# Kernel optimization log

Hardware: AMD Instinct MI355X
Metric: run time of the kernel (lower is better)

## Reference

```python
import jax, jax.numpy as jnp
import numpy as np

N, D, L, OUT, E = 50000, 64, 3, 16, 800000


def setup_inputs() -> dict:
    key = jax.random.key(0)
    ks = jax.random.split(key, 7)
    F = jax.random.normal(ks[0], (N, D), dtype=jnp.float32)
    src = jax.random.randint(ks[1], (E,), 0, N, dtype=jnp.int32)
    dst = jax.random.randint(ks[2], (E,), 0, N, dtype=jnp.int32)
    gcn_w = jax.random.normal(ks[3], (L, D, D), dtype=jnp.float32) / np.float32(np.sqrt(D))
    gcn_b = jnp.zeros((L, D), dtype=jnp.float32)
    fc_w = jax.random.normal(ks[4], (OUT, N * D), dtype=jnp.float32) / np.float32(np.sqrt(N * D))
    fc_b = jnp.zeros((OUT,), dtype=jnp.float32)
    return {"F": F, "src": src, "dst": dst, "gcn_w": gcn_w, "gcn_b": gcn_b,
            "fc_w": fc_w, "fc_b": fc_b}


def reference(F, src, dst, gcn_w, gcn_b, fc_w, fc_b):
    n = F.shape[0]
    # dgl.add_self_loop: append a self edge for every node
    loops = jnp.arange(n, dtype=src.dtype)
    s = jnp.concatenate([src, loops])
    d = jnp.concatenate([dst, loops])
    ones = jnp.ones(s.shape[0], dtype=F.dtype)
    deg_out = jax.ops.segment_sum(ones, s, num_segments=n)  # out-degree of src
    deg_in = jax.ops.segment_sum(ones, d, num_segments=n)   # in-degree of dst
    # self loops guarantee deg >= 1
    norm_src = deg_out ** -0.5
    norm_dst = deg_in ** -0.5
    x = F
    for i in range(gcn_w.shape[0]):
        h = x * norm_src[:, None]                              # [N, D]
        agg = jax.ops.segment_sum(h[s], d, num_segments=n)     # SpMM gather-scatter
        x = (agg * norm_dst[:, None]) @ gcn_w[i] + gcn_b[i]    # GraphConv norm='both'
        x = jax.nn.relu(x)
    flat = jax.nn.relu(x.reshape(-1))                          # Flatten(start_dim=0) + ReLU
    return fc_w @ flat + fc_b                                  # [OUT]
```

## Files before the change

kernel.cpp:

```cpp
#include <hip/hip_runtime.h>
#include <cstdint>

#define Nn 50000
#define Dd 64
#define Ee 800000
#define NBLK 196
#define FC_BLOCKS 512
#define ND4 (Nn*Dd/4)
#define NDTOT ((size_t)Nn * 64)

__device__ __forceinline__ float relu_f(float v){ return v > 0.f ? v : 0.f; }

__device__ __forceinline__ unsigned short f2bf(float f){
    unsigned u = __float_as_uint(f);
    u += 0x7fffu + ((u >> 16) & 1u);
    return (unsigned short)(u >> 16);
}
__device__ __forceinline__ void add_bf8(float* a, uint4 u){
    a[0] += __uint_as_float(u.x << 16);
    a[1] += __uint_as_float(u.x & 0xffff0000u);
    a[2] += __uint_as_float(u.y << 16);
    a[3] += __uint_as_float(u.y & 0xffff0000u);
    a[4] += __uint_as_float(u.z << 16);
    a[5] += __uint_as_float(u.z & 0xffff0000u);
    a[6] += __uint_as_float(u.w << 16);
    a[7] += __uint_as_float(u.w & 0xffff0000u);
}
__device__ __forceinline__ int rowidx(unsigned e, unsigned end, const unsigned* __restrict__ csr){
    unsigned ec = e < (Ee - 1u) ? e : (Ee - 1u);
    int idx = (int)csr[ec];
    return (e < end) ? idx : Nn;
}

__global__ __launch_bounds__(256) void k_degree(const int* __restrict__ src, const int* __restrict__ dst,
                                                unsigned* __restrict__ dout, unsigned* __restrict__ din){
    int e = blockIdx.x * 256 + threadIdx.x;
    if (e < Ee){
        atomicAdd(&dout[src[e]], 1u);
        atomicAdd(&din[dst[e]], 1u);
    }
}

__global__ __launch_bounds__(256) void k_blocksum(const unsigned* __restrict__ din, const unsigned* __restrict__ dout,
                                                  unsigned* __restrict__ bsum,
                                                  float* __restrict__ ns, float* __restrict__ nd){
    __shared__ unsigned s[256];
    int t = threadIdx.x; int i = blockIdx.x * 256 + t;
    unsigned v = (i < Nn) ? din[i] : 0u;
    s[t] = v;
    if (i < Nn){
        ns[i] = rsqrtf((float)(dout[i] + 1u));
        nd[i] = rsqrtf((float)(v + 1u));
    }
    __syncthreads();
    for (int off = 128; off > 0; off >>= 1){ if (t < off) s[t] += s[t + off]; __syncthreads(); }
    if (t == 0) bsum[blockIdx.x] = s[0];
}

__global__ __launch_bounds__(256) void k_scanblocks(const unsigned* __restrict__ bsum, unsigned* __restrict__ boff,
                                                    unsigned* __restrict__ offsets){
    __shared__ unsigned s[256];
    int t = threadIdx.x;
    unsigned v = (t < NBLK) ? bsum[t] : 0u;
    s[t] = v; __syncthreads();
    for (int off = 1; off < 256; off <<= 1){
        unsigned add = (t >= off) ? s[t - off] : 0u;
        __syncthreads();
        s[t] += add;
        __syncthreads();
    }
    boff[t] = s[t] - v;
    if (t == 255) offsets[Nn] = s[255];
}

__global__ __launch_bounds__(256) void k_offsets(const unsigned* __restrict__ din, const unsigned* __restrict__ boff,
                                                 unsigned* __restrict__ offsets, unsigned* __restrict__ cursor){
    __shared__ unsigned s[256];
    int t = threadIdx.x; int i = blockIdx.x * 256 + t;
    unsigned v = (i < Nn) ? din[i] : 0u;
    s[t] = v; __syncthreads();
    for (int off = 1; off < 256; off <<= 1){
        unsigned add = (t >= off) ? s[t - off] : 0u;
        __syncthreads();
        s[t] += add;
        __syncthreads();
    }
    if (i < Nn){
        unsigned val = s[t] - v + boff[blockIdx.x];
        offsets[i] = val;
        cursor[i]  = val;
    }
}

__global__ __launch_bounds__(256) void k_fillcsr(const int* __restrict__ src, const int* __restrict__ dst,
                                                 unsigned* __restrict__ cursor, unsigned* __restrict__ csr){
    int e = blockIdx.x * 256 + threadIdx.x;
    if (e < Ee){
        unsigned pos = atomicAdd(&cursor[dst[e]], 1u);
        csr[pos] = (unsigned)src[e];
    }
}

__global__ __launch_bounds__(256) void k_h0(const float* __restrict__ x, const float* __restrict__ ns,
                                            unsigned short* __restrict__ hA, unsigned short* __restrict__ hB){
    int i = blockIdx.x * 256 + threadIdx.x;
    if (i < ND4){
        const float4* x4 = (const float4*)x;
        float s = ns[i >> 4];
        float4 v = x4[i];
        ushort4 o;
        o.x = f2bf(v.x * s); o.y = f2bf(v.y * s);
        o.z = f2bf(v.z * s); o.w = f2bf(v.w * s);
        ((ushort4*)hA)[i] = o;
    } else {
        int j = i - ND4;
        if (j < 16){
            ushort4 z = make_ushort4(0, 0, 0, 0);
            ((ushort4*)hA)[ND4 + j] = z;
            ((ushort4*)hB)[ND4 + j] = z;
        }
    }
}

__global__ __launch_bounds__(256) void k_gather(const unsigned short* __restrict__ h,
                                                const unsigned* __restrict__ offsets,
                                                const unsigned* __restrict__ csr, const float* __restrict__ nd,
                                                float* __restrict__ agg){
    int v = blockIdx.x * 4 + (threadIdx.x >> 6);
    int lane = threadIdx.x & 63;
    int slot = lane >> 3;
    int sub  = lane & 7;
    const uint4* h16 = (const uint4*)h;

    unsigned beg = offsets[v], end = offsets[v + 1];
    unsigned e0 = beg + slot;

    int i0 = rowidx(e0,      end, csr);
    int i1 = rowidx(e0 + 8,  end, csr);
    int i2 = rowidx(e0 + 16, end, csr);
    int i3 = rowidx(e0 + 24, end, csr);
    uint4 u0 = h16[(size_t)i0 * 8 + sub];
    uint4 u1 = h16[(size_t)i1 * 8 + sub];
    uint4 u2 = h16[(size_t)i2 * 8 + sub];
    uint4 u3 = h16[(size_t)i3 * 8 + sub];

    float acc[8];
    #pragma unroll
    for (int i = 0; i < 8; i++) acc[i] = 0.f;
    if (slot == 0) add_bf8(acc, h16[(size_t)v * 8 + sub]);
    add_bf8(acc, u0);
    add_bf8(acc, u1);
    add_bf8(acc, u2);
    add_bf8(acc, u3);

    for (unsigned e = e0 + 32; e < end; e += 8){
        add_bf8(acc, h16[(size_t)((int)csr[e]) * 8 + sub]);
    }

    #pragma unroll
    for (int i = 0; i < 8; i++) acc[i] += __shfl_xor(acc[i], 8, 64);
    #pragma unroll
    for (int i = 0; i < 8; i++) acc[i] += __shfl_xor(acc[i], 16, 64);
    #pragma unroll
    for (int i = 0; i < 8; i++) acc[i] += __shfl_xor(acc[i], 32, 64);

    if (slot == 0){
        float s = nd[v];
        float4* aggp = (float4*)agg;
        aggp[(size_t)v * 16 + sub * 2 + 0] = make_float4(acc[0] * s, acc[1] * s, acc[2] * s, acc[3] * s);
        aggp[(size_t)v * 16 + sub * 2 + 1] = make_float4(acc[4] * s, acc[5] * s, acc[6] * s, acc[7] * s);
    }
}

__global__ __launch_bounds__(256) void k_gemm(const float* __restrict__ agg, const float* __restrict__ W,
                                              const float* __restrict__ bias, const float* __restrict__ ns,
                                              void* __restrict__ xout, int bf16_prescale_out){
    __shared__ float As[64 * 65];
    __shared__ float Ws[64 * 64];
    int t = threadIdx.x;
    int m_base = blockIdx.x * 64;
    const float4* W4   = (const float4*)W;
    float4* Ws4        = (float4*)Ws;
    const float4* agg4 = (const float4*)agg;
    #pragma unroll
    for (int i = 0; i < 4; i++){
        int g = t + 256 * i;
        Ws4[g] = W4[g];
        int m = g >> 4, q = g & 15;
        int node = m_base + m;
        float4 v = make_float4(0.f, 0.f, 0.f, 0.f);
        if (node < Nn) v = agg4[node * 16 + q];
        float* dp = &As[m * 65 + q * 4];
        dp[0] = v.x; dp[1] = v.y; dp[2] = v.z; dp[3] = v.w;
    }
    __syncthreads();
    int tm = t >> 4, tn = t & 15;
    float acc[4][4];
    #pragma unroll
    for (int i = 0; i < 4; i++)
        #pragma unroll
        for (int j = 0; j < 4; j++) acc[i][j] = 0.f;
    #pragma unroll 4
    for (int k = 0; k < 64; k++){
        float4 w = *(const float4*)&Ws[k * 64 + tn * 4];
        float a[4];
        #pragma unroll
        for (int i = 0; i < 4; i++) a[i] = As[(tm * 4 + i) * 65 + k];
        #pragma unroll
        for (int i = 0; i < 4; i++){
            acc[i][0] += a[i] * w.x;
            acc[i][1] += a[i] * w.y;
            acc[i][2] += a[i] * w.z;
            acc[i][3] += a[i] * w.w;
        }
    }
    float4 b4 = ((const float4*)bias)[tn];
    #pragma unroll
    for (int i = 0; i < 4; i++){
        int node = m_base + tm * 4 + i;
        if (node < Nn){
            float4 r;
            r.x = relu_f(acc[i][0] + b4.x);
            r.y = relu_f(acc[i][1] + b4.y);
            r.z = relu_f(acc[i][2] + b4.z);
            r.w = relu_f(acc[i][3] + b4.w);
            if (bf16_prescale_out){
                float s = ns[node];
                ushort4 o;
                o.x = f2bf(r.x * s); o.y = f2bf(r.y * s);
                o.z = f2bf(r.z * s); o.w = f2bf(r.w * s);
                ((ushort4*)xout)[node * 16 + tn] = o;
            } else {
                ((float4*)xout)[node * 16 + tn] = r;
            }
        }
    }
}

__global__ __launch_bounds__(256) void k_fc(const float* __restrict__ fcw, const float* __restrict__ x,
                                            float* __restrict__ partials){
    int t = threadIdx.x;
    const float4* x4 = (const float4*)x;
    const float4* w4 = (const float4*)fcw;
    float p[16];
    #pragma unroll
    for (int o = 0; o < 16; o++) p[o] = 0.f;
    for (int i = blockIdx.x * 256 + t; i < ND4; i += FC_BLOCKS * 256){
        float4 xv = x4[i];
        #pragma unroll
        for (int o = 0; o < 16; o++){
            float4 wv = w4[(size_t)o * ND4 + i];
            p[o] += wv.x * xv.x + wv.y * xv.y + wv.z * xv.z + wv.w * xv.w;
        }
    }
    #pragma unroll
    for (int o = 0; o < 16; o++){
        for (int off = 32; off > 0; off >>= 1) p[o] += __shfl_down(p[o], off, 64);
    }
    __shared__ float red[4][16];
    int lane = t & 63, wid = t >> 6;
    if (lane == 0){
        #pragma unroll
        for (int o = 0; o < 16; o++) red[wid][o] = p[o];
    }
    __syncthreads();
    if (t < 16) partials[blockIdx.x * 16 + t] = red[0][t] + red[1][t] + red[2][t] + red[3][t];
}

__global__ __launch_bounds__(256) void k_fc2(const float* __restrict__ partials, const float* __restrict__ fcb,
                                             float* __restrict__ out){
    __shared__ float red[256];
    int t = threadIdx.x; int o = t & 15, j0 = t >> 4;
    float s = 0.f;
    for (int j = j0; j < FC_BLOCKS; j += 16) s += partials[j * 16 + o];
    red[t] = s; __syncthreads();
    for (int off = 128; off >= 16; off >>= 1){ if (t < off) red[t] += red[t + off]; __syncthreads(); }
    if (t < 16) out[t] = red[t] + fcb[t];
}

extern "C" void kernel_launch(void* const* d_in, const int* in_sizes, int n_in,
                              void* d_out, int out_size, void* d_ws, size_t ws_size,
                              hipStream_t stream) {
    const float* F     = (const float*)d_in[0];
    const int*   src   = (const int*)d_in[1];
    const int*   dst   = (const int*)d_in[2];
    const float* gcn_w = (const float*)d_in[3];
    const float* gcn_b = (const float*)d_in[4];
    const float* fc_w  = (const float*)d_in[5];
    const float* fc_b  = (const float*)d_in[6];
    float* out = (float*)d_out;

    char* wsp = (char*)d_ws;
    auto alloc = [&](size_t bytes) -> char* {
        char* p = wsp;
        wsp += (bytes + 255) & ~size_t(255);
        return p;
    };
    unsigned* deg      = (unsigned*)alloc(2 * Nn * 4);
    unsigned* deg_out_ = deg;
    unsigned* deg_in_  = deg + Nn;
    unsigned* offsets  = (unsigned*)alloc((Nn + 1) * 4);
    unsigned* cursor   = (unsigned*)alloc(Nn * 4);
    unsigned* bsum     = (unsigned*)alloc(256 * 4);
    unsigned* boff     = (unsigned*)alloc(256 * 4);
    unsigned* csr      = (unsigned*)alloc(Ee * 4);
    float* norm_src    = (float*)alloc(Nn * 4);
    float* norm_dst    = (float*)alloc(Nn * 4);
    float* partials    = (float*)alloc(FC_BLOCKS * 16 * 4);
    unsigned short* hA = (unsigned short*)alloc((NDTOT + 64) * 2);
    unsigned short* hB = (unsigned short*)alloc((NDTOT + 64) * 2);
    float* aggb        = (float*)alloc(NDTOT * 4);
    float* xf          = (float*)alloc(NDTOT * 4);

    hipMemsetAsync(deg, 0, 2 * Nn * 4, stream);

    k_degree<<<Ee / 256, 256, 0, stream>>>(src, dst, deg_out_, deg_in_);
    k_blocksum<<<NBLK, 256, 0, stream>>>(deg_in_, deg_out_, bsum, norm_src, norm_dst);
    k_scanblocks<<<1, 256, 0, stream>>>(bsum, boff, offsets);
    k_offsets<<<NBLK, 256, 0, stream>>>(deg_in_, boff, offsets, cursor);
    k_fillcsr<<<Ee / 256, 256, 0, stream>>>(src, dst, cursor, csr);

    k_h0<<<ND4 / 256 + 1, 256, 0, stream>>>(F, norm_src, hA, hB);

    int nblk_gemm = (Nn + 63) / 64;
    k_gather<<<Nn / 4, 256, 0, stream>>>(hA, offsets, csr, norm_dst, aggb);
    k_gemm<<<nblk_gemm, 256, 0, stream>>>(aggb, gcn_w + 0 * 4096, gcn_b + 0 * 64, norm_src, hB, 1);
    k_gather<<<Nn / 4, 256, 0, stream>>>(hB, offsets, csr, norm_dst, aggb);
    k_gemm<<<nblk_gemm, 256, 0, stream>>>(aggb, gcn_w + 1 * 4096, gcn_b + 1 * 64, norm_src, hA, 1);
    k_gather<<<Nn / 4, 256, 0, stream>>>(hA, offsets, csr, norm_dst, aggb);
    k_gemm<<<nblk_gemm, 256, 0, stream>>>(aggb, gcn_w + 2 * 4096, gcn_b + 2 * 64, norm_src, xf, 0);

    k_fc<<<FC_BLOCKS, 256, 0, stream>>>(fc_w, xf, partials);
    k_fc2<<<1, 256, 0, stream>>>(partials, fc_b, out);
}
```

Before: 540.8 us.

## Store aggregates in bf16 and fuse final GEMM with FC reduction

The gather kernel now writes normalized aggregates as bf16 instead of fp32, and the GEMM kernels read and convert them. The last layer's GEMM is fused with the fully-connected projection, computing per-block partial dot products against fc_w directly. This removes the fp32 intermediate activation buffer and its write and read. The cost is an extra bf16 rounding step on the aggregates, plus a per-block shared-memory reduction in the fused kernel.

```diff
diff --git a/kernel.cpp b/kernel.cpp
--- a/kernel.cpp
+++ b/kernel.cpp
@@ -2,12 +2,11 @@
 #include <cstdint>
 
 #define Nn 50000
-#define Dd 64
 #define Ee 800000
 #define NBLK 196
-#define FC_BLOCKS 512
-#define ND4 (Nn*Dd/4)
+#define ND4 (Nn*64/4)
 #define NDTOT ((size_t)Nn * 64)
+#define NGB 782
 
 __device__ __forceinline__ float relu_f(float v){ return v > 0.f ? v : 0.f; }
 
@@ -15,6 +14,9 @@
     unsigned u = __float_as_uint(f);
     u += 0x7fffu + ((u >> 16) & 1u);
     return (unsigned short)(u >> 16);
+}
+__device__ __forceinline__ float bf2f(unsigned short s){
+    return __uint_as_float((unsigned)s << 16);
 }
 __device__ __forceinline__ void add_bf8(float* a, uint4 u){
     a[0] += __uint_as_float(u.x << 16);
@@ -125,7 +127,7 @@
 __global__ __launch_bounds__(256) void k_gather(const unsigned short* __restrict__ h,
                                                 const unsigned* __restrict__ offsets,
                                                 const unsigned* __restrict__ csr, const float* __restrict__ nd,
-                                                float* __restrict__ agg){
+                                                unsigned short* __restrict__ agg){
     int v = blockIdx.x * 4 + (threadIdx.x >> 6);
     int lane = threadIdx.x & 63;
     int slot = lane >> 3;
@@ -166,32 +168,37 @@
 
     if (slot == 0){
         float s = nd[v];
-        float4* aggp = (float4*)agg;
-        aggp[(size_t)v * 16 + sub * 2 + 0] = make_float4(acc[0] * s, acc[1] * s, acc[2] * s, acc[3] * s);
-        aggp[(size_t)v * 16 + sub * 2 + 1] = make_float4(acc[4] * s, acc[5] * s, acc[6] * s, acc[7] * s);
-    }
-}
-
-__global__ __launch_bounds__(256) void k_gemm(const float* __restrict__ agg, const float* __restrict__ W,
+        ushort4 o0, o1;
+        o0.x = f2bf(acc[0] * s); o0.y = f2bf(acc[1] * s);
+        o0.z = f2bf(acc[2] * s); o0.w = f2bf(acc[3] * s);
+        o1.x = f2bf(acc[4] * s); o1.y = f2bf(acc[5] * s);
+        o1.z = f2bf(acc[6] * s); o1.w = f2bf(acc[7] * s);
+        ushort4* aggp = (ushort4*)agg;
+        aggp[(size_t)v * 16 + sub * 2 + 0] = o0;
+        aggp[(size_t)v * 16 + sub * 2 + 1] = o1;
+    }
+}
+
+__global__ __launch_bounds__(256) void k_gemm(const unsigned short* __restrict__ agg, const float* __restrict__ W,
                                               const float* __restrict__ bias, const float* __restrict__ ns,
-                                              void* __restrict__ xout, int bf16_prescale_out){
+                                              unsigned short* __restrict__ xout){
     __shared__ float As[64 * 65];
     __shared__ float Ws[64 * 64];
     int t = threadIdx.x;
     int m_base = blockIdx.x * 64;
-    const float4* W4   = (const float4*)W;
-    float4* Ws4        = (float4*)Ws;
-    const float4* agg4 = (const float4*)agg;
+    const float4* W4  = (const float4*)W;
+    float4* Ws4       = (float4*)Ws;
+    const ushort4* a4 = (const ushort4*)agg;
     #pragma unroll
     for (int i = 0; i < 4; i++){
         int g = t + 256 * i;
         Ws4[g] = W4[g];
         int m = g >> 4, q = g & 15;
         int node = m_base + m;
-        float4 v = make_float4(0.f, 0.f, 0.f, 0.f);
-        if (node < Nn) v = agg4[node * 16 + q];
+        ushort4 u = make_ushort4(0, 0, 0, 0);
+        if (node < Nn) u = a4[(size_t)node * 16 + q];
         float* dp = &As[m * 65 + q * 4];
-        dp[0] = v.x; dp[1] = v.y; dp[2] = v.z; dp[3] = v.w;
+        dp[0] = bf2f(u.x); dp[1] = bf2f(u.y); dp[2] = bf2f(u.z); dp[3] = bf2f(u.w);
     }
     __syncthreads();
     int tm = t >> 4, tn = t & 15;
@@ -219,60 +226,103 @@
     for (int i = 0; i < 4; i++){
         int node = m_base + tm * 4 + i;
         if (node < Nn){
-            float4 r;
-            r.x = relu_f(acc[i][0] + b4.x);
-            r.y = relu_f(acc[i][1] + b4.y);
-            r.z = relu_f(acc[i][2] + b4.z);
-            r.w = relu_f(acc[i][3] + b4.w);
-            if (bf16_prescale_out){
-                float s = ns[node];
-                ushort4 o;
-                o.x = f2bf(r.x * s); o.y = f2bf(r.y * s);
-                o.z = f2bf(r.z * s); o.w = f2bf(r.w * s);
-                ((ushort4*)xout)[node * 16 + tn] = o;
-            } else {
-                ((float4*)xout)[node * 16 + tn] = r;
-            }
-        }
-    }
-}
-
-__global__ __launch_bounds__(256) void k_fc(const float* __restrict__ fcw, const float* __restrict__ x,
-                                            float* __restrict__ partials){
+            float s = ns[node];
+            ushort4 o;
+            o.x = f2bf(relu_f(acc[i][0] + b4.x) * s);
+            o.y = f2bf(relu_f(acc[i][1] + b4.y) * s);
+            o.z = f2bf(relu_f(acc[i][2] + b4.z) * s);
+            o.w = f2bf(relu_f(acc[i][3] + b4.w) * s);
+            ((ushort4*)xout)[(size_t)node * 16 + tn] = o;
+        }
+    }
+}
+
+__global__ __launch_bounds__(256) void k_gemm2fc(const unsigned short* __restrict__ agg, const float* __restrict__ W,
+                                                 const float* __restrict__ bias, const float* __restrict__ fcw,
+                                                 float* __restrict__ partials){
+    __shared__ float As[64 * 65];
+    __shared__ float Ws[64 * 64];
     int t = threadIdx.x;
-    const float4* x4 = (const float4*)x;
-    const float4* w4 = (const float4*)fcw;
+    int m_base = blockIdx.x * 64;
+    const float4* W4  = (const float4*)W;
+    float4* Ws4       = (float4*)Ws;
+    const ushort4* a4 = (const ushort4*)agg;
+    #pragma unroll
+    for (int i = 0; i < 4; i++){
+        int g = t + 256 * i;
+        Ws4[g] = W4[g];
+        int m = g >> 4, q = g & 15;
+        int node = m_base + m;
+        ushort4 u = make_ushort4(0, 0, 0, 0);
+        if (node < Nn) u = a4[(size_t)node * 16 + q];
+        float* dp = &As[m * 65 + q * 4];
+        dp[0] = bf2f(u.x); dp[1] = bf2f(u.y); dp[2] = bf2f(u.z); dp[3] = bf2f(u.w);
+    }
+    __syncthreads();
+    int tm = t >> 4, tn = t & 15;
+    float acc[4][4];
+    #pragma unroll
+    for (int i = 0; i < 4; i++)
+        #pragma unroll
+        for (int j = 0; j < 4; j++) acc[i][j] = 0.f;
+    #pragma unroll 4
+    for (int k = 0; k < 64; k++){
+        float4 w = *(const float4*)&Ws[k * 64 + tn * 4];
+        float a[4];
+        #pragma unroll
+        for (int i = 0; i < 4; i++) a[i] = As[(tm * 4 + i) * 65 + k];
+        #pragma unroll
+        for (int i = 0; i < 4; i++){
+            acc[i][0] += a[i] * w.x;
+            acc[i][1] += a[i] * w.y;
+            acc[i][2] += a[i] * w.z;
+            acc[i][3] += a[i] * w.w;
+        }
+    }
+    float4 b4 = ((const float4*)bias)[tn];
+    #pragma unroll
+    for (int i = 0; i < 4; i++){
+        acc[i][0] = relu_f(acc[i][0] + b4.x);
+        acc[i][1] = relu_f(acc[i][1] + b4.y);
+        acc[i][2] = relu_f(acc[i][2] + b4.z);
+        acc[i][3] = relu_f(acc[i][3] + b4.w);
+    }
+    const float4* fw4 = (const float4*)fcw;
     float p[16];
     #pragma unroll
-    for (int o = 0; o < 16; o++) p[o] = 0.f;
-    for (int i = blockIdx.x * 256 + t; i < ND4; i += FC_BLOCKS * 256){
-        float4 xv = x4[i];
-        #pragma unroll
-        for (int o = 0; o < 16; o++){
-            float4 wv = w4[(size_t)o * ND4 + i];
-            p[o] += wv.x * xv.x + wv.y * xv.y + wv.z * xv.z + wv.w * xv.w;
-        }
-    }
-    #pragma unroll
     for (int o = 0; o < 16; o++){
-        for (int off = 32; off > 0; off >>= 1) p[o] += __shfl_down(p[o], off, 64);
-    }
-    __shared__ float red[4][16];
-    int lane = t & 63, wid = t >> 6;
-    if (lane == 0){
-        #pragma unroll
-        for (int o = 0; o < 16; o++) red[wid][o] = p[o];
-    }
-    __syncthreads();
-    if (t < 16) partials[blockIdx.x * 16 + t] = red[0][t] + red[1][t] + red[2][t] + red[3][t];
+        float s = 0.f;
+        #pragma unroll
+        for (int i = 0; i < 4; i++){
+            int node = m_base + tm * 4 + i;
+            int nc = node < Nn ? node : (Nn - 1);
+            float4 w = fw4[(size_t)o * ND4 + (size_t)nc * 16 + tn];
+            float m = (node < Nn) ? 1.f : 0.f;
+            s += m * (acc[i][0] * w.x + acc[i][1] * w.y + acc[i][2] * w.z + acc[i][3] * w.w);
+        }
+        p[o] = s;
+    }
+    __syncthreads();
+    #pragma unroll
+    for (int o = 0; o < 16; o++) Ws[o * 256 + t] = p[o];
+    __syncthreads();
+    int o = t >> 4, i2 = t & 15;
+    float s = 0.f;
+    #pragma unroll
+    for (int m = 0; m < 16; m++) s += Ws[o * 256 + m * 16 + i2];
+    s += __shfl_down(s, 8, 64);
+    s += __shfl_down(s, 4, 64);
+    s += __shfl_down(s, 2, 64);
+    s += __shfl_down(s, 1, 64);
+    if (i2 == 0) partials[blockIdx.x * 16 + o] = s;
 }
 
 __global__ __launch_bounds__(256) void k_fc2(const float* __restrict__ partials, const float* __restrict__ fcb,
                                              float* __restrict__ out){
     __shared__ float red[256];
-    int t = threadIdx.x; int o = t & 15, j0 = t >> 4;
+    int t = threadIdx.x; int o = t & 15, rr = t >> 4;
     float s = 0.f;
-    for (int j = j0; j < FC_BLOCKS; j += 16) s += partials[j * 16 + o];
+    for (int r = rr; r < NGB; r += 16) s += partials[r * 16 + o];
     red[t] = s; __syncthreads();
     for (int off = 128; off >= 16; off >>= 1){ if (t < off) red[t] += red[t + off]; __syncthreads(); }
     if (t < 16) out[t] = red[t] + fcb[t];
@@ -306,11 +356,10 @@
     unsigned* csr      = (unsigned*)alloc(Ee * 4);
     float* norm_src    = (float*)alloc(Nn * 4);
     float* norm_dst    = (float*)alloc(Nn * 4);
-    float* partials    = (float*)alloc(FC_BLOCKS * 16 * 4);
+    float* partials    = (float*)alloc(NGB * 16 * 4);
     unsigned short* hA = (unsigned short*)alloc((NDTOT + 64) * 2);
     unsigned short* hB = (unsigned short*)alloc((NDTOT + 64) * 2);
-    float* aggb        = (float*)alloc(NDTOT * 4);
-    float* xf          = (float*)alloc(NDTOT * 4);
+    unsigned short* aggb = (unsigned short*)alloc(NDTOT * 2);
 
     hipMemsetAsync(deg, 0, 2 * Nn * 4, stream);
 
@@ -322,14 +371,12 @@
 
     k_h0<<<ND4 / 256 + 1, 256, 0, stream>>>(F, norm_src, hA, hB);
 
-    int nblk_gemm = (Nn + 63) / 64;
     k_gather<<<Nn / 4, 256, 0, stream>>>(hA, offsets, csr, norm_dst, aggb);
-    k_gemm<<<nblk_gemm, 256, 0, stream>>>(aggb, gcn_w + 0 * 4096, gcn_b + 0 * 64, norm_src, hB, 1);
+    k_gemm<<<NGB, 256, 0, stream>>>(aggb, gcn_w + 0 * 4096, gcn_b + 0 * 64, norm_src, hB);
     k_gather<<<Nn / 4, 256, 0, stream>>>(hB, offsets, csr, norm_dst, aggb);
-    k_gemm<<<nblk_gemm, 256, 0, stream>>>(aggb, gcn_w + 1 * 4096, gcn_b + 1 * 64, norm_src, hA, 1);
+    k_gemm<<<NGB, 256, 0, stream>>>(aggb, gcn_w + 1 * 4096, gcn_b + 1 * 64, norm_src, hA);
     k_gather<<<Nn / 4, 256, 0, stream>>>(hA, offsets, csr, norm_dst, aggb);
-    k_gemm<<<nblk_gemm, 256, 0, stream>>>(aggb, gcn_w + 2 * 4096, gcn_b + 2 * 64, norm_src, xf, 0);
-
-    k_fc<<<FC_BLOCKS, 256, 0, stream>>>(fc_w, xf, partials);
+    k_gemm2fc<<<NGB, 256, 0, stream>>>(aggb, gcn_w + 2 * 4096, gcn_b + 2 * 64, fc_w, partials);
+
     k_fc2<<<1, 256, 0, stream>>>(partials, fc_b, out);
 }
```

Result: no change. 545.2 us (+0.8%).
